# Kernel tuning notes

Measured on AMD Instinct MI355X. Metric: run time of the kernel, lower is better.

Reference implementation:

```python
import jax, jax.numpy as jnp
import numpy as np

NUM_CLASSES = 1      # hard-coded in panoptic_inference2
MASK_THR = 1e-3      # cur_masks[:, k] >= 0.001


def _panoptic_single(logits, mask_logits, pad):
    # logits: [Q, C+1], mask_logits: [P, Q], pad: [P] bool (all False here)
    scores = logits.max(axis=-1)                      # cur_scores per query
    labels = jnp.argmax(logits, axis=-1)              # predicted class per query
    keep = labels != NUM_CLASSES                      # drop 'no-object' queries

    m = jax.nn.sigmoid(mask_logits)                   # [P, Q] cur_masks
    prob_masks = scores[None, :] * m                  # cur_prob_masks [P, Q]
    # emulate column selection cur_masks[:, keep] by masking with -inf
    masked = jnp.where(keep[None, :], prob_masks, -jnp.inf)

    # probabilities = softmax over (kept) queries; max_confs = per-point max prob
    soft = jax.nn.softmax(masked, axis=1)             # [P, Q]
    max_confs = soft.max(axis=1)                      # [P]

    # cur_mask_ids = argmax over kept queries (indices in full query space)
    mid = jnp.argmax(masked, axis=1)                  # [P]
    m_sel = jnp.take_along_axis(m, mid[:, None], axis=1)[:, 0]
    # point contributes to segment k iff argmax==k AND sigmoid>=thr (and not padded)
    valid = (m_sel >= MASK_THR) & (~pad) & keep[mid]  # [P]

    Q = logits.shape[0]
    # per-query area of mask = (mid==k) & thr ; segment kept iff nonempty
    counts = jnp.zeros((Q,), jnp.int32).at[mid].add(valid.astype(jnp.int32))
    nonempty = counts > 0
    # sequential segment ids in query order (masks are disjoint, so the
    # conf-based reordering in the original cannot change sem/ins)
    seg_id = jnp.cumsum(nonempty.astype(jnp.int32))   # [Q]

    ins = jnp.where(valid, seg_id[mid], 0).astype(jnp.int32)
    sem = jnp.where(valid, labels[mid].astype(jnp.int32), 0)
    return sem, ins, max_confs


def setup_inputs() -> dict:
    key = jax.random.key(0)
    k1, k2 = jax.random.split(key)
    B, P, Q, C1 = 2, 200000, 100, NUM_CLASSES + 1
    pred_logits = jax.random.normal(k1, (B, Q, C1), dtype=jnp.float32)
    pred_masks = jax.random.normal(k2, (B, P, Q), dtype=jnp.float32)
    padding = jnp.zeros((B, P), dtype=bool)
    return {"pred_logits": pred_logits, "pred_masks": pred_masks, "padding": padding}


def reference(pred_logits, pred_masks, padding):
    sem, ins, max_confs = jax.vmap(_panoptic_single)(pred_logits, pred_masks, padding)
    return sem, ins, max_confs
```

## Files before the change

kernel.cpp:

```cpp
#include <hip/hip_runtime.h>
#include <math.h>

#define B_   2
#define P_   200000
#define Q_   100
#define NREP 64


__global__ void pano_prep(const float* __restrict__ logits,
                          float* __restrict__ msc)
{
    const int b = blockIdx.x, tid = threadIdx.x;
    if (tid < Q_) {
        float l0 = logits[(b * Q_ + tid) * 2 + 0];
        float l1 = logits[(b * Q_ + tid) * 2 + 1];
        msc[b * Q_ + tid] = (l1 > l0) ? -1e30f : fmaxf(l0, l1);
    }
}

__global__ __launch_bounds__(256) void pano_pass1(
    const float* __restrict__ masks,
    const unsigned char* __restrict__ pad,
    float* __restrict__ out,
    const float* __restrict__ msc,
    int* __restrict__ flags)
{
    const int b = blockIdx.y, tid = threadIdx.x;
    __shared__ float s_msc[Q_];
    __shared__ int   s_flag[Q_];
    if (tid < Q_) { s_msc[tid] = msc[b * Q_ + tid]; s_flag[tid] = 0; }
    __syncthreads();

    const int wave = tid >> 6, wl = tid & 63;
    const int g = wl >> 2, l = wl & 3;
    const int p = blockIdx.x * 64 + wave * 16 + g;

    const float* rowp = masks + ((size_t)b * P_ + p) * Q_;
    const float4* grow = reinterpret_cast<const float4*>(rowp);

    float4 v[7];
    #pragma unroll
    for (int k = 0; k < 6; ++k) v[k] = grow[k * 4 + l];
    v[6] = grow[24];

    float S0 = 0.0f;
    float v1 = -INFINITY, v2 = -INFINITY, m1 = 0.0f;
    int   q1 = -1;

    #pragma unroll
    for (int k = 0; k < 7; ++k) {
        const bool act = (k < 6) || (l == 0);
        const int  qb  = (k < 6) ? (16 * k + 4 * l) : 96;
        float xv[4] = {v[k].x, v[k].y, v[k].z, v[k].w};
        #pragma unroll
        for (int e = 0; e < 4; ++e) {
            int q = qb + e;
            float m   = __builtin_amdgcn_rcpf(1.0f + __expf(-xv[e]));
            float val = act ? s_msc[q] * m : -INFINITY;
            S0 += __expf(val);
            bool t = val > v1;
            v2 = t ? v1 : fmaxf(v2, val);
            v1 = t ? val : v1;
            m1 = t ? m   : m1;
            q1 = t ? q   : q1;
        }
    }

    #pragma unroll
    for (int off = 1; off <= 2; off <<= 1) {
        float So  = __shfl_xor(S0, off, 64);
        float v1o = __shfl_xor(v1, off, 64);
        float v2o = __shfl_xor(v2, off, 64);
        float m1o = __shfl_xor(m1, off, 64);
        int   q1o = __shfl_xor(q1, off, 64);
        S0 += So;
        bool t = (v1o > v1) || (v1o == v1 && (unsigned)q1o < (unsigned)q1);
        v2 = fmaxf(fminf(v1, v1o), fmaxf(v2, v2o));
        v1 = t ? v1o : v1;
        m1 = t ? m1o : m1;
        q1 = t ? q1o : q1;
    }

    if (l == 0 && (v1 - v2) < 5e-5f) {
        float bv = -INFINITY, bm = 0.0f; int bq = -1;
        for (int q = 0; q < Q_; ++q) {
            float x = rowp[q];
            float e = expf(-x);
            float m = 1.0f / (1.0f + e);
            float vv = s_msc[q] * m;
            if (vv > bv) { bv = vv; bq = q; bm = m; }
        }
        q1 = bq; m1 = bm;
    }

    bool valid = (q1 >= 0) && (s_msc[q1] > -1e29f) &&
                 (m1 >= 1e-3f) &&
                 (pad[(size_t)b * P_ + p] == 0);

    float conf = __expf(v1) * __builtin_amdgcn_rcpf(S0);
    float insf = valid ? (float)q1 : -1.0f;
    if (l == 0 && valid) s_flag[q1] = 1;

    int   src    = (wl & 15) * 4;
    float conf_g = __shfl(conf, src, 64);
    float insf_g = __shfl(insf, src, 64);
    if (wl < 16) {
        int prow = blockIdx.x * 64 + wave * 16 + wl;
        size_t o = (size_t)b * P_ + prow;
        out[o]                       = 0.0f;
        out[(size_t)B_ * P_ + o]     = insf_g;
        out[2 * (size_t)B_ * P_ + o] = conf_g;
    }

    __syncthreads();
    if (tid < Q_ && s_flag[tid]) {
        int rep = blockIdx.x & (NREP - 1);
        atomicOr(&flags[(b * NREP + rep) * Q_ + tid], 1);
    }
}

__global__ void pano_pass2(const int* __restrict__ flags,
                           int* __restrict__ seg)
{
    const int b = blockIdx.x, tid = threadIdx.x;
    __shared__ int s_ne[Q_];
    if (tid < Q_) {
        int f = 0;
        for (int r = 0; r < NREP; ++r)
            f |= flags[(b * NREP + r) * Q_ + tid];
        s_ne[tid] = f ? 1 : 0;
    }
    __syncthreads();
    if (tid == 0) {
        int c = 0;
        #pragma unroll
        for (int q = 0; q < Q_; ++q) { c += s_ne[q]; s_ne[q] = c; }
    }
    __syncthreads();
    if (tid < Q_) seg[b * Q_ + tid] = s_ne[tid];
}

__global__ __launch_bounds__(256) void pano_pass3(
    const int* __restrict__ seg,
    float* __restrict__ out)
{
    const int b = blockIdx.y, tid = threadIdx.x;
    __shared__ int s_seg[Q_];
    if (tid < Q_) s_seg[tid] = seg[b * Q_ + tid];
    __syncthreads();

    int p = blockIdx.x * blockDim.x + tid;
    if (p < P_) {
        size_t o = (size_t)B_ * P_ + (size_t)b * P_ + p;
        float f = out[o];
        out[o] = (f >= 0.0f) ? (float)s_seg[(int)f] : 0.0f;
    }
}

extern "C" void kernel_launch(void* const* d_in, const int* in_sizes, int n_in,
                              void* d_out, int out_size, void* d_ws, size_t ws_size,
                              hipStream_t stream) {
    const float* logits = (const float*)d_in[0];
    const float* masks  = (const float*)d_in[1];
    const unsigned char* pad = (const unsigned char*)d_in[2];
    float* out = (float*)d_out;

    int*   flags = (int*)d_ws;
    float* mscp  = (float*)((char*)d_ws + 52224);
    int*   seg   = (int*)((char*)d_ws + 53248);

    hipMemsetAsync(d_ws, 0, B_ * NREP * Q_ * sizeof(int), stream);
    pano_prep<<<dim3(B_), dim3(128), 0, stream>>>(logits, mscp);

    dim3 block(256);
    pano_pass1<<<dim3(P_ / 64, B_), block, 0, stream>>>(masks, pad, out, mscp, flags);
    pano_pass2<<<dim3(B_), dim3(128), 0, stream>>>(flags, seg);
    pano_pass3<<<dim3((P_ + 255) / 256, B_), block, 0, stream>>>(seg, out);
}
```

Baseline: 246.9 us.

## Pack nonempty flags into bitmasks and fold memset and pass2 into other kernels

```diff
diff --git a/kernel.cpp b/kernel.cpp
--- a/kernel.cpp
+++ b/kernel.cpp
@@ -8,13 +8,16 @@
 
 
 __global__ void pano_prep(const float* __restrict__ logits,
-                          float* __restrict__ msc)
+                          float* __restrict__ msc,
+                          unsigned int* __restrict__ flags32)
 {
-    const int b = blockIdx.x, tid = threadIdx.x;
-    if (tid < Q_) {
-        float l0 = logits[(b * Q_ + tid) * 2 + 0];
-        float l1 = logits[(b * Q_ + tid) * 2 + 1];
-        msc[b * Q_ + tid] = (l1 > l0) ? -1e30f : fmaxf(l0, l1);
+    const int tid = threadIdx.x;
+    flags32[tid]       = 0u;
+    flags32[tid + 256] = 0u;
+    if (tid < B_ * Q_) {
+        float l0 = logits[tid * 2 + 0];
+        float l1 = logits[tid * 2 + 1];
+        msc[tid] = (l1 > l0) ? -1e30f : fmaxf(l0, l1);
     }
 }
 
@@ -23,7 +26,7 @@
     const unsigned char* __restrict__ pad,
     float* __restrict__ out,
     const float* __restrict__ msc,
-    int* __restrict__ flags)
+    unsigned long long* __restrict__ flags)
 {
     const int b = blockIdx.y, tid = threadIdx.x;
     __shared__ float s_msc[Q_];
@@ -113,43 +116,39 @@
     }
 
     __syncthreads();
-    if (tid < Q_ && s_flag[tid]) {
-        int rep = blockIdx.x & (NREP - 1);
-        atomicOr(&flags[(b * NREP + rep) * Q_ + tid], 1);
+    if (wave < 2) {
+        bool pred = (tid < Q_) && (s_flag[tid] != 0);
+        unsigned long long mbits = __ballot(pred);
+        if (wl == 0 && mbits) {
+            int rep = blockIdx.x & (NREP - 1);
+            atomicOr(&flags[((size_t)b * NREP + rep) * 2 + wave], mbits);
+        }
     }
 }
 
-__global__ void pano_pass2(const int* __restrict__ flags,
-                           int* __restrict__ seg)
+__global__ __launch_bounds__(256) void pano_pass23(
+    const unsigned int* __restrict__ flags32,
+    float* __restrict__ out)
 {
-    const int b = blockIdx.x, tid = threadIdx.x;
-    __shared__ int s_ne[Q_];
-    if (tid < Q_) {
-        int f = 0;
-        for (int r = 0; r < NREP; ++r)
-            f |= flags[(b * NREP + r) * Q_ + tid];
-        s_ne[tid] = f ? 1 : 0;
-    }
+    const int b = blockIdx.y, tid = threadIdx.x;
+    __shared__ unsigned int s_bits[4];
+    __shared__ int s_seg[Q_];
+    if (tid < 4) s_bits[tid] = 0u;
+    __syncthreads();
+    unsigned int w = flags32[b * 256 + tid];
+    if (w) atomicOr(&s_bits[tid & 3], w);
     __syncthreads();
     if (tid == 0) {
         int c = 0;
         #pragma unroll
-        for (int q = 0; q < Q_; ++q) { c += s_ne[q]; s_ne[q] = c; }
+        for (int q = 0; q < Q_; ++q) {
+            c += (s_bits[q >> 5] >> (q & 31)) & 1;
+            s_seg[q] = c;
+        }
     }
     __syncthreads();
-    if (tid < Q_) seg[b * Q_ + tid] = s_ne[tid];
-}
 
-__global__ __launch_bounds__(256) void pano_pass3(
-    const int* __restrict__ seg,
-    float* __restrict__ out)
-{
-    const int b = blockIdx.y, tid = threadIdx.x;
-    __shared__ int s_seg[Q_];
-    if (tid < Q_) s_seg[tid] = seg[b * Q_ + tid];
-    __syncthreads();
-
-    int p = blockIdx.x * blockDim.x + tid;
+    int p = blockIdx.x * 256 + tid;
     if (p < P_) {
         size_t o = (size_t)B_ * P_ + (size_t)b * P_ + p;
         float f = out[o];
@@ -165,15 +164,11 @@
     const unsigned char* pad = (const unsigned char*)d_in[2];
     float* out = (float*)d_out;
 
-    int*   flags = (int*)d_ws;
-    float* mscp  = (float*)((char*)d_ws + 52224);
-    int*   seg   = (int*)((char*)d_ws + 53248);
+    unsigned long long* flags   = (unsigned long long*)d_ws;
+    unsigned int*       flags32 = (unsigned int*)d_ws;
+    float*              mscp    = (float*)((char*)d_ws + 2048);
 
-    hipMemsetAsync(d_ws, 0, B_ * NREP * Q_ * sizeof(int), stream);
-    pano_prep<<<dim3(B_), dim3(128), 0, stream>>>(logits, mscp);
-
-    dim3 block(256);
-    pano_pass1<<<dim3(P_ / 64, B_), block, 0, stream>>>(masks, pad, out, mscp, flags);
-    pano_pass2<<<dim3(B_), dim3(128), 0, stream>>>(flags, seg);
-    pano_pass3<<<dim3((P_ + 255) / 256, B_), block, 0, stream>>>(seg, out);
+    pano_prep<<<dim3(1), dim3(256), 0, stream>>>(logits, mscp, flags32);
+    pano_pass1<<<dim3(P_ / 64, B_), dim3(256), 0, stream>>>(masks, pad, out, mscp, flags);
+    pano_pass23<<<dim3((P_ + 255) / 256, B_), dim3(256), 0, stream>>>(flags32, out);
 }
```

Result: faster. 240.2 us (-2.7%).
